# Optimization experiments

Measured on AMD Instinct MI355X. Metric: run time of the kernel, lower is better.

Reference implementation:

```python
import jax, jax.numpy as jnp
import numpy as np

T, D_IN, D_H, D_OUT = 16384, 1024, 1024, 1024
SCALE = 0.03  # keep tanh out of deep saturation


def setup_inputs() -> dict:
    key = jax.random.key(0)
    ks = jax.random.split(key, 6)
    return {
        "X_seq": jax.random.normal(ks[0], (T, D_IN), dtype=jnp.float32),
        "Wx": jax.random.normal(ks[1], (D_IN, D_H), dtype=jnp.float32) * SCALE,
        "Wh": jax.random.normal(ks[2], (D_H, D_H), dtype=jnp.float32) * SCALE,
        "Wy": jax.random.normal(ks[3], (D_H, D_OUT), dtype=jnp.float32) * SCALE,
        "bh": jax.random.normal(ks[4], (D_H,), dtype=jnp.float32) * SCALE,
        "by": jax.random.normal(ks[5], (D_OUT,), dtype=jnp.float32) * SCALE,
    }


def reference(X_seq, Wx, Wh, Wy, bh, by):
    # Vanilla RNN: h_t = tanh(x_t @ Wx + h_{t-1} @ Wh + bh); y_t = h_t @ Wy + by.
    # The torch code skips the Wh term at t=0, which equals using h_{-1} = 0.
    h0 = jnp.zeros((Wx.shape[1],), dtype=X_seq.dtype)

    def step(h_prev, x_t):
        h = jnp.tanh(x_t @ Wx + h_prev @ Wh + bh)
        y = h @ Wy + by
        return h, (h, y)

    _, (hidden, outputs) = jax.lax.scan(step, h0, X_seq)
    return (hidden, outputs)  # each [T, 1024]
```

## Files before the change

kernel.cpp:

```cpp
#include <hip/hip_runtime.h>
#include <cstdint>
#include <cstddef>

constexpr int T_STEPS = 16384;
constexpr int D = 1024;
constexpr int G_WG = 64;
constexpr int C_COLS = 16;

typedef __attribute__((ext_vector_type(8))) short bf16x8;
typedef __attribute__((ext_vector_type(4))) float f32x4;

__device__ unsigned long long g_hpub[2 * D];

static __device__ __forceinline__ unsigned short f2bf(float f) {
  union { float f; unsigned int u; } v;
  v.f = f;
  unsigned int u = v.u;
  unsigned int r = (u + 0x7fffu + ((u >> 16) & 1u)) >> 16;
  return (unsigned short)r;
}
static __device__ __forceinline__ unsigned int f_as_u(float f) {
  union { float f; unsigned int u; } v; v.f = f; return v.u;
}
static __device__ __forceinline__ float u_as_f(unsigned int u) {
  union { unsigned int u; float f; } v; v.u = u; return v.f;
}

__global__ void init_hpub() {
  const int i = blockIdx.x * 256 + threadIdx.x;
  if (i < 2 * D) g_hpub[i] = 0ull;
}

__global__ __launch_bounds__(256, 2) void gemm_bias(
    const float* __restrict__ A, const float* __restrict__ B,
    const float* __restrict__ bias, float* __restrict__ out, int M, int N,
    int K) {
  const int tid = threadIdx.x;
  const int wave = tid >> 6;
  const int lane = tid & 63;
  const int lrow = lane & 15;
  const int quad = lane >> 4;
  const int m0 = blockIdx.x * 64;
  const int n0 = blockIdx.y * 64;

  __shared__ __align__(16) unsigned short sA[64][40];
  __shared__ __align__(16) unsigned short sB[32][68];

  f32x4 acc[4];
#pragma unroll
  for (int s = 0; s < 4; ++s) acc[s] = (f32x4){0.f, 0.f, 0.f, 0.f};

  const int ar = tid >> 2;
  const int ac = (tid & 3) * 8;
  const int br = tid >> 3;
  const int bc = (tid & 7) * 8;

  for (int k0 = 0; k0 < K; k0 += 32) {
    union { unsigned short u[8]; uint4 v; } apk, bpk;
    {
      const float4 a0 = *(const float4*)(A + (size_t)(m0 + ar) * K + k0 + ac);
      const float4 a1 = *(const float4*)(A + (size_t)(m0 + ar) * K + k0 + ac + 4);
      apk.u[0] = f2bf(a0.x); apk.u[1] = f2bf(a0.y);
      apk.u[2] = f2bf(a0.z); apk.u[3] = f2bf(a0.w);
      apk.u[4] = f2bf(a1.x); apk.u[5] = f2bf(a1.y);
      apk.u[6] = f2bf(a1.z); apk.u[7] = f2bf(a1.w);
      const float4 b0 = *(const float4*)(B + (size_t)(k0 + br) * N + n0 + bc);
      const float4 b1 = *(const float4*)(B + (size_t)(k0 + br) * N + n0 + bc + 4);
      bpk.u[0] = f2bf(b0.x); bpk.u[1] = f2bf(b0.y);
      bpk.u[2] = f2bf(b0.z); bpk.u[3] = f2bf(b0.w);
      bpk.u[4] = f2bf(b1.x); bpk.u[5] = f2bf(b1.y);
      bpk.u[6] = f2bf(b1.z); bpk.u[7] = f2bf(b1.w);
    }

    __syncthreads();
    *(uint4*)&sA[ar][ac] = apk.v;
    *(uint2*)&sB[br][bc] = make_uint2(bpk.v.x, bpk.v.y);
    *(uint2*)&sB[br][bc + 4] = make_uint2(bpk.v.z, bpk.v.w);
    __syncthreads();

    bf16x8 afrag = *(const bf16x8*)&sA[16 * wave + lrow][quad * 8];
#pragma unroll
    for (int s = 0; s < 4; ++s) {
      bf16x8 bfrag;
#pragma unroll
      for (int jj = 0; jj < 8; ++jj)
        bfrag[jj] = (short)sB[quad * 8 + jj][s * 16 + lrow];
      acc[s] = __builtin_amdgcn_mfma_f32_16x16x32_bf16(afrag, bfrag, acc[s], 0, 0, 0);
    }
  }

#pragma unroll
  for (int s = 0; s < 4; ++s) {
    const int col = n0 + s * 16 + lrow;
    const float bsv = bias[col];
#pragma unroll
    for (int r = 0; r < 4; ++r) {
      const int row = m0 + 16 * wave + quad * 4 + r;
      out[(size_t)row * N + col] = acc[s][r] + bsv;
    }
  }
}

__global__ __launch_bounds__(256, 1) void rnn_recur(
    const float* __restrict__ Apre, const float* __restrict__ Wh,
    float* __restrict__ Hout) {
  const int g = blockIdx.x;
  const int tid = threadIdx.x;
  const int j = tid & 15;
  const int rc = tid >> 4;
  const int col = g * C_COLS + j;
  const int wave = tid >> 6;
  const int lane = tid & 63;

  float W[64];
#pragma unroll
  for (int kk = 0; kk < 64; ++kk)
    W[kk] = Wh[(size_t)(rc * 64 + kk) * D + col];

  __shared__ float hl[D];
  __shared__ int sdead;
  __shared__ float red[64];
  if (tid == 0) sdead = 0;
  for (int i = tid; i < D; i += 256) hl[i] = 0.f;
  __syncthreads();

  float acur = Apre[col];
  int dead = 0;

  for (int t = 0; t < T_STEPS; ++t) {
    float anext = 0.f;
    if (t + 1 < T_STEPS) anext = Apre[(size_t)(t + 1) * D + col];

    float accv = 0.f;
    const float4* hv = (const float4*)&hl[rc * 64];
#pragma unroll
    for (int kk = 0; kk < 16; ++kk) {
      float4 h4 = hv[kk];
      accv = fmaf(W[4 * kk + 0], h4.x, accv);
      accv = fmaf(W[4 * kk + 1], h4.y, accv);
      accv = fmaf(W[4 * kk + 2], h4.z, accv);
      accv = fmaf(W[4 * kk + 3], h4.w, accv);
    }
    accv += __shfl_xor(accv, 16);
    accv += __shfl_xor(accv, 32);
    if (lane < 16) red[wave * 16 + lane] = accv;
    __syncthreads();

    if (tid < 16) {
      float pre = acur + red[j] + red[16 + j] + red[32 + j] + red[48 + j];
      pre = fminf(fmaxf(pre, -30.f), 30.f);
      float h = tanhf(pre);
      Hout[(size_t)t * D + col] = h;
      const unsigned long long pk =
          ((unsigned long long)(unsigned)(t + 1) << 32) |
          (unsigned long long)f_as_u(h);
      __hip_atomic_store(&g_hpub[(t & 1) * D + col], pk, __ATOMIC_RELAXED,
                         __HIP_MEMORY_SCOPE_AGENT);
    }

    acur = anext;
    if (t + 1 == T_STEPS) break;

    if (!dead) {
      const unsigned int want = (unsigned)(t + 1);
      const int base = (t & 1) * D + tid * 4;
      int pend = 0xF;
      int spins = 0;
      do {
#pragma unroll
        for (int q = 0; q < 4; ++q) {
          if (pend & (1 << q)) {
            unsigned long long w = __hip_atomic_load(
                &g_hpub[base + q], __ATOMIC_RELAXED, __HIP_MEMORY_SCOPE_AGENT);
            if ((unsigned)(w >> 32) == want) {
              hl[tid * 4 + q] = u_as_f((unsigned)w);
              pend &= ~(1 << q);
            }
          }
        }
        if (!pend) break;
        if ((++spins & 7) == 7) __builtin_amdgcn_s_sleep(1);
        if (spins > (1 << 20)) { sdead = 1; break; }
      } while (true);
    }
    __syncthreads();
    dead |= sdead;
  }
}

extern "C" void kernel_launch(void* const* d_in, const int* in_sizes, int n_in,
                              void* d_out, int out_size, void* d_ws,
                              size_t ws_size, hipStream_t stream) {
  const float* X  = (const float*)d_in[0];
  const float* Wx = (const float*)d_in[1];
  const float* Wh = (const float*)d_in[2];
  const float* Wy = (const float*)d_in[3];
  const float* bh = (const float*)d_in[4];
  const float* by = (const float*)d_in[5];

  float* Hout = (float*)d_out;
  float* Yout = Hout + (size_t)T_STEPS * D;
  float* Apre = Yout;

  const dim3 ggrid(T_STEPS / 64, D / 64);

  init_hpub<<<dim3((2 * D + 255) / 256), dim3(256), 0, stream>>>();

  gemm_bias<<<ggrid, dim3(256), 0, stream>>>(X, Wx, bh, Apre, T_STEPS, D, D);

  rnn_recur<<<dim3(G_WG), dim3(256), 0, stream>>>(Apre, Wh, Hout);

  gemm_bias<<<ggrid, dim3(256), 0, stream>>>(Hout, Wy, by, Yout, T_STEPS, D, D);
}
```

Baseline: 39.34 ms.

## Reduce per-wave via shuffles, drop a barrier, double-buffer padded hidden state

Remaps threads so each wave owns four output columns and finishes the dot-product reduction with lane shuffles. This removes the shared-memory reduction and one __syncthreads per timestep. The hidden-state buffer is double-buffered and padded to avoid bank conflicts. Each block writes its own new h values locally and skips polling its own slots. The poll loop now issues four unconditional loads per iteration and sleeps less often, targeting per-step latency on the serial recurrence critical path.

```diff
diff --git a/kernel.cpp b/kernel.cpp
--- a/kernel.cpp
+++ b/kernel.cpp
@@ -106,22 +106,21 @@
     float* __restrict__ Hout) {
   const int g = blockIdx.x;
   const int tid = threadIdx.x;
-  const int j = tid & 15;
-  const int rc = tid >> 4;
-  const int col = g * C_COLS + j;
   const int wave = tid >> 6;
   const int lane = tid & 63;
+  const int j4 = lane & 3;
+  const int rc = lane >> 2;
+  const int col = g * C_COLS + wave * 4 + j4;
 
   float W[64];
 #pragma unroll
   for (int kk = 0; kk < 64; ++kk)
     W[kk] = Wh[(size_t)(rc * 64 + kk) * D + col];
 
-  __shared__ float hl[D];
+  __shared__ __align__(16) float hlp[2][16 * 68];
   __shared__ int sdead;
-  __shared__ float red[64];
   if (tid == 0) sdead = 0;
-  for (int i = tid; i < D; i += 256) hl[i] = 0.f;
+  for (int i = tid; i < 2 * 16 * 68; i += 256) ((float*)hlp)[i] = 0.f;
   __syncthreads();
 
   float acur = Apre[col];
@@ -132,7 +131,7 @@
     if (t + 1 < T_STEPS) anext = Apre[(size_t)(t + 1) * D + col];
 
     float accv = 0.f;
-    const float4* hv = (const float4*)&hl[rc * 64];
+    const float4* hv = (const float4*)&hlp[t & 1][rc * 68];
 #pragma unroll
     for (int kk = 0; kk < 16; ++kk) {
       float4 h4 = hv[kk];
@@ -141,47 +140,51 @@
       accv = fmaf(W[4 * kk + 2], h4.z, accv);
       accv = fmaf(W[4 * kk + 3], h4.w, accv);
     }
+    accv += __shfl_xor(accv, 4);
+    accv += __shfl_xor(accv, 8);
     accv += __shfl_xor(accv, 16);
     accv += __shfl_xor(accv, 32);
-    if (lane < 16) red[wave * 16 + lane] = accv;
-    __syncthreads();
-
-    if (tid < 16) {
-      float pre = acur + red[j] + red[16 + j] + red[32 + j] + red[48 + j];
+
+    if (lane < 4) {
+      float pre = acur + accv;
       pre = fminf(fmaxf(pre, -30.f), 30.f);
-      float h = tanhf(pre);
-      Hout[(size_t)t * D + col] = h;
+      const float h = tanhf(pre);
       const unsigned long long pk =
           ((unsigned long long)(unsigned)(t + 1) << 32) |
           (unsigned long long)f_as_u(h);
       __hip_atomic_store(&g_hpub[(t & 1) * D + col], pk, __ATOMIC_RELAXED,
                          __HIP_MEMORY_SCOPE_AGENT);
+      Hout[(size_t)t * D + col] = h;
+      hlp[(t + 1) & 1][col + (col >> 6) * 4] = h;
     }
 
     acur = anext;
     if (t + 1 == T_STEPS) break;
 
-    if (!dead) {
+    if (!dead && (tid >> 2) != g) {
       const unsigned int want = (unsigned)(t + 1);
       const int base = (t & 1) * D + tid * 4;
-      int pend = 0xF;
+      unsigned long long w0, w1, w2, w3;
       int spins = 0;
       do {
-#pragma unroll
-        for (int q = 0; q < 4; ++q) {
-          if (pend & (1 << q)) {
-            unsigned long long w = __hip_atomic_load(
-                &g_hpub[base + q], __ATOMIC_RELAXED, __HIP_MEMORY_SCOPE_AGENT);
-            if ((unsigned)(w >> 32) == want) {
-              hl[tid * 4 + q] = u_as_f((unsigned)w);
-              pend &= ~(1 << q);
-            }
-          }
-        }
-        if (!pend) break;
-        if ((++spins & 7) == 7) __builtin_amdgcn_s_sleep(1);
+        w0 = __hip_atomic_load(&g_hpub[base + 0], __ATOMIC_RELAXED,
+                               __HIP_MEMORY_SCOPE_AGENT);
+        w1 = __hip_atomic_load(&g_hpub[base + 1], __ATOMIC_RELAXED,
+                               __HIP_MEMORY_SCOPE_AGENT);
+        w2 = __hip_atomic_load(&g_hpub[base + 2], __ATOMIC_RELAXED,
+                               __HIP_MEMORY_SCOPE_AGENT);
+        w3 = __hip_atomic_load(&g_hpub[base + 3], __ATOMIC_RELAXED,
+                               __HIP_MEMORY_SCOPE_AGENT);
+        if (((unsigned)(w0 >> 32) == want) & ((unsigned)(w1 >> 32) == want) &
+            ((unsigned)(w2 >> 32) == want) & ((unsigned)(w3 >> 32) == want))
+          break;
+        if ((++spins & 15) == 15) __builtin_amdgcn_s_sleep(1);
         if (spins > (1 << 20)) { sdead = 1; break; }
       } while (true);
+      const int hb = 4 * tid + 4 * (tid >> 4);
+      *(float4*)&hlp[(t + 1) & 1][hb] =
+          make_float4(u_as_f((unsigned)w0), u_as_f((unsigned)w1),
+                      u_as_f((unsigned)w2), u_as_f((unsigned)w3));
     }
     __syncthreads();
     dead |= sdead;
```

Result: slower. 48.39 ms (+23.0%).
